# Performance work log

Measured on AMD Instinct MI355X. Metric: run time of the kernel, lower is better.

## Reference

```python
import jax, jax.numpy as jnp
import numpy as np

BS = 8192
NUM_CLASSES = 400
D = 768


def _bilin_from_14(m14, Y, X, eH, eW):
    # Value of bilinear-resize(m14 -> (eH,eW)) at integer pixel (Y,X), computed on the fly.
    # torch F.interpolate(align_corners=False): src = (dst+0.5)*in/out - 0.5, clamped at 0.
    # m14: (bs,14,14); Y,X: (bs,14) float integer-valued coords; eH,eW: (bs,) float.
    sy = jnp.maximum((Y + 0.5) * 14.0 / eH[:, None] - 0.5, 0.0)
    sx = jnp.maximum((X + 0.5) * 14.0 / eW[:, None] - 0.5, 0.0)
    r0f = jnp.floor(sy); c0f = jnp.floor(sx)
    r0 = r0f.astype(jnp.int32); r1 = jnp.minimum(r0 + 1, 13)
    c0 = c0f.astype(jnp.int32); c1 = jnp.minimum(c0 + 1, 13)
    fy = sy - r0f; fx = sx - c0f
    b = jnp.arange(m14.shape[0])[:, None, None]
    g00 = m14[b, r0[:, :, None], c0[:, None, :]]
    g01 = m14[b, r0[:, :, None], c1[:, None, :]]
    g10 = m14[b, r1[:, :, None], c0[:, None, :]]
    g11 = m14[b, r1[:, :, None], c1[:, None, :]]
    wy = fy[:, :, None]; wx = fx[:, None, :]
    return g00 * (1 - wy) * (1 - wx) + g01 * (1 - wy) * wx + g10 * wy * (1 - wx) + g11 * wy * wx


def _get_mask(attn, o_pos, e_pos):
    # Fused, fully-batched equivalent of the per-sample python loop:
    #   resize 14x14 -> (eH,eW) bilinear; crop (top,left,oH,oW); resize -> 14x14 bilinear.
    # The final resize only reads the intermediate grid at 4 integer points per output
    # pixel, so we evaluate those points lazily via _bilin_from_14 (exact, no Emax grid).
    bs = attn.shape[0]
    m14 = attn.reshape(bs, 14, 14)
    eH = e_pos[:, 2].astype(jnp.float32); eW = e_pos[:, 3].astype(jnp.float32)
    top = (o_pos[:, 0] - e_pos[:, 0]).astype(jnp.float32)
    left = (o_pos[:, 1] - e_pos[:, 1]).astype(jnp.float32)
    oH = o_pos[:, 2].astype(jnp.float32); oW = o_pos[:, 3].astype(jnp.float32)
    i = jnp.arange(14, dtype=jnp.float32)[None, :]
    ty = jnp.maximum((i + 0.5) * oH[:, None] / 14.0 - 0.5, 0.0)  # (bs,14) coords in crop
    tx = jnp.maximum((i + 0.5) * oW[:, None] / 14.0 - 0.5, 0.0)
    y0 = jnp.floor(ty); y1 = jnp.minimum(y0 + 1.0, oH[:, None] - 1.0); wy = ty - y0
    x0 = jnp.floor(tx); x1 = jnp.minimum(x0 + 1.0, oW[:, None] - 1.0); wx = tx - x0
    Y0 = top[:, None] + y0; Y1 = top[:, None] + y1  # absolute rows in (eH,eW) grid
    X0 = left[:, None] + x0; X1 = left[:, None] + x1
    v00 = _bilin_from_14(m14, Y0, X0, eH, eW)
    v01 = _bilin_from_14(m14, Y0, X1, eH, eW)
    v10 = _bilin_from_14(m14, Y1, X0, eH, eW)
    v11 = _bilin_from_14(m14, Y1, X1, eH, eW)
    wyc = wy[:, :, None]; wxc = wx[:, None, :]
    out = v00 * (1 - wyc) * (1 - wxc) + v01 * (1 - wyc) * wxc + v10 * wyc * (1 - wxc) + v11 * wyc * wxc
    return out.reshape(bs, 196)


def _get_att_mask(attention, ratio=0.5):
    bs = attention.shape[0]
    a14 = attention.reshape(bs, 14, 14)
    # bilinear 14->7 with align_corners=False samples at frac 0.5 == 2x2 average pool
    a7 = a14.reshape(bs, 7, 2, 7, 2).mean(axis=(2, 4))
    flat = a7.reshape(bs, 49)
    n_keep = int(49 * ratio) + 1  # argsort desc, take top N+1 = 25
    _, idx = jax.lax.top_k(flat, n_keep)
    masks = jnp.ones((bs, 49), dtype=bool)
    masks = masks.at[jnp.arange(bs)[:, None], idx].set(False)
    m7 = masks.reshape(bs, 7, 7)
    full = jnp.repeat(jnp.repeat(m7, 2, axis=1), 2, axis=2)
    return full.reshape(bs, 196)


def setup_inputs() -> dict:
    key = jax.random.key(0)
    k1, k2, k3 = jax.random.split(key, 3)
    attn = jax.random.uniform(k1, (BS, 196), dtype=jnp.float32)
    rng = np.random.default_rng(0)
    IMG = 224
    eH = rng.integers(112, IMG + 1, BS); eW = rng.integers(112, IMG + 1, BS)
    eT = rng.integers(0, IMG - eH + 1); eL = rng.integers(0, IMG - eW + 1)
    def box():
        h = rng.integers(56, eH + 1); w = rng.integers(56, eW + 1)
        t = eT + rng.integers(0, eH - h + 1); l = eL + rng.integers(0, eW - w + 1)
        return np.stack([t, l, h, w], axis=1)
    e = np.stack([eT, eL, eH, eW], axis=1)
    pos = np.stack([box(), box(), e], axis=1).astype(np.int32)  # (BS,3,4)
    image_embed = jax.random.normal(k2, (2 * BS, D), dtype=jnp.float32)
    W = jax.random.normal(k3, (NUM_CLASSES, D), dtype=jnp.float32) * 0.02
    b = jnp.zeros((NUM_CLASSES,), dtype=jnp.float32)
    return {"attn": attn, "pos": jnp.asarray(pos), "image_embed": image_embed, "W": W, "b": b}


def reference(attn, pos, image_embed, W, b):
    cm1 = _get_mask(attn, pos[:, 0], pos[:, 2])
    mask1 = _get_att_mask(cm1)
    cm2 = _get_mask(attn, pos[:, 1], pos[:, 2])
    mask2 = _get_att_mask(cm2)
    mask = jnp.concatenate([mask1, mask2], axis=0)  # (2*bs,196) bool, fed to masked encoder
    logits = image_embed @ W.T + b
    return logits, mask
```

## Files before the change

kernel.cpp:

```cpp
#include <hip/hip_runtime.h>
#include <hip/hip_bf16.h>

#define BSAMP 8192
#define NCLS 400
#define DIM 768
#define MROWS 16384
#define LOGITS_SIZE (16384LL * 400LL)

typedef __attribute__((ext_vector_type(8))) short short8;
typedef __attribute__((ext_vector_type(4))) float floatx4;

__device__ inline unsigned short f2bf(float f) {
    unsigned int u = __float_as_uint(f);
    return (unsigned short)((u + 0x7FFFu + ((u >> 16) & 1u)) >> 16);
}

__device__ inline uint4 pack8(float4 a, float4 b) {
    union { unsigned short u[8]; uint4 v; } p;
    p.u[0] = f2bf(a.x); p.u[1] = f2bf(a.y); p.u[2] = f2bf(a.z); p.u[3] = f2bf(a.w);
    p.u[4] = f2bf(b.x); p.u[5] = f2bf(b.y); p.u[6] = f2bf(b.z); p.u[7] = f2bf(b.w);
    return p.v;
}

__global__ __launch_bounds__(256) void gemm_kernel(const float* __restrict__ E,
                                                   const float* __restrict__ W,
                                                   const float* __restrict__ bias,
                                                   float* __restrict__ out) {
    __shared__ __align__(16) unsigned short sA[128 * 32];
    __shared__ __align__(16) unsigned short sB[80 * 32];

    const int t    = threadIdx.x;
    const int n0   = blockIdx.x * 80;
    const int m0   = blockIdx.y * 128;
    const int wave = t >> 6;
    const int lane = t & 63;
    const int quad = lane >> 4;
    const int l16  = lane & 15;

    const int aRow = t >> 1;
    const int aCol = (t & 1) * 16;
    const float* aSrc = E + (size_t)(m0 + aRow) * DIM + aCol;
    const float* bSrc = W + (size_t)(n0 + aRow) * DIM + aCol;

    floatx4 acc[2][5];
#pragma unroll
    for (int mi = 0; mi < 2; ++mi)
#pragma unroll
        for (int ni = 0; ni < 5; ++ni)
            acc[mi][ni] = (floatx4){0.f, 0.f, 0.f, 0.f};

    for (int k0 = 0; k0 < DIM; k0 += 32) {
        {
            const float4* s = (const float4*)(aSrc + k0);
            float4 f0 = s[0], f1 = s[1], f2 = s[2], f3 = s[3];
            *(uint4*)&sA[aRow * 32 + aCol]     = pack8(f0, f1);
            *(uint4*)&sA[aRow * 32 + aCol + 8] = pack8(f2, f3);
        }
        if (t < 160) {
            const float4* s = (const float4*)(bSrc + k0);
            float4 f0 = s[0], f1 = s[1], f2 = s[2], f3 = s[3];
            *(uint4*)&sB[aRow * 32 + aCol]     = pack8(f0, f1);
            *(uint4*)&sB[aRow * 32 + aCol + 8] = pack8(f2, f3);
        }
        __syncthreads();

        short8 af0 = *(const short8*)&sA[(wave * 32 + l16) * 32 + quad * 8];
        short8 af1 = *(const short8*)&sA[(wave * 32 + 16 + l16) * 32 + quad * 8];
#pragma unroll
        for (int ni = 0; ni < 5; ++ni) {
            short8 bf = *(const short8*)&sB[(ni * 16 + l16) * 32 + quad * 8];
            acc[0][ni] = __builtin_amdgcn_mfma_f32_16x16x32_bf16(af0, bf, acc[0][ni], 0, 0, 0);
            acc[1][ni] = __builtin_amdgcn_mfma_f32_16x16x32_bf16(af1, bf, acc[1][ni], 0, 0, 0);
        }
        __syncthreads();
    }

#pragma unroll
    for (int ni = 0; ni < 5; ++ni) {
        int col = n0 + ni * 16 + l16;
        float bv = bias[col];
#pragma unroll
        for (int mi = 0; mi < 2; ++mi) {
            int rowBase = m0 + wave * 32 + mi * 16 + quad * 4;
#pragma unroll
            for (int r = 0; r < 4; ++r) {
                out[(size_t)(rowBase + r) * NCLS + col] = acc[mi][ni][r] + bv;
            }
        }
    }
}

__device__ inline float bilin14(const float* m14, float Y, float X, float eH, float eW) {
    float sy = fmaxf((Y + 0.5f) * 14.0f / eH - 0.5f, 0.0f);
    float sx = fmaxf((X + 0.5f) * 14.0f / eW - 0.5f, 0.0f);
    float r0f = floorf(sy);
    float c0f = floorf(sx);
    int r0 = (int)r0f;
    int r1 = min(r0 + 1, 13);
    int c0 = (int)c0f;
    int c1 = min(c0 + 1, 13);
    float fy = sy - r0f;
    float fx = sx - c0f;
    float g00 = m14[r0 * 14 + c0];
    float g01 = m14[r0 * 14 + c1];
    float g10 = m14[r1 * 14 + c0];
    float g11 = m14[r1 * 14 + c1];
    return g00 * (1.f - fy) * (1.f - fx) + g01 * (1.f - fy) * fx +
           g10 * fy * (1.f - fx) + g11 * fy * fx;
}

__global__ __launch_bounds__(64) void mask_kernel(const float* __restrict__ attn,
                                                  const int* __restrict__ pos,
                                                  float* __restrict__ out_mask) {
    const int p = blockIdx.x;
    const int b = p & (BSAMP - 1);
    const int o = p >> 13;
    const int t = threadIdx.x;

    __shared__ float m14[196];
    __shared__ float a7[49];

    for (int i = t; i < 196; i += 64) m14[i] = attn[(size_t)b * 196 + i];

    const int* pb = pos + (size_t)b * 12;
    const float top  = (float)(pb[o * 4 + 0] - pb[8]);
    const float left = (float)(pb[o * 4 + 1] - pb[9]);
    const float oH   = (float)pb[o * 4 + 2];
    const float oW   = (float)pb[o * 4 + 3];
    const float eH   = (float)pb[10];
    const float eW   = (float)pb[11];
    __syncthreads();

    int i7 = t / 7, j7 = t % 7;
    if (t < 49) {
        float s = 0.f;
#pragma unroll
        for (int dy = 0; dy < 2; ++dy) {
            int oy = 2 * i7 + dy;
            float ty = fmaxf((oy + 0.5f) * oH / 14.0f - 0.5f, 0.0f);
            float y0 = floorf(ty);
            float y1 = fminf(y0 + 1.0f, oH - 1.0f);
            float wy = ty - y0;
            float Y0 = top + y0, Y1 = top + y1;
#pragma unroll
            for (int dx = 0; dx < 2; ++dx) {
                int ox = 2 * j7 + dx;
                float tx = fmaxf((ox + 0.5f) * oW / 14.0f - 0.5f, 0.0f);
                float x0 = floorf(tx);
                float x1 = fminf(x0 + 1.0f, oW - 1.0f);
                float wx = tx - x0;
                float X0 = left + x0, X1 = left + x1;
                float v00 = bilin14(m14, Y0, X0, eH, eW);
                float v01 = bilin14(m14, Y0, X1, eH, eW);
                float v10 = bilin14(m14, Y1, X0, eH, eW);
                float v11 = bilin14(m14, Y1, X1, eH, eW);
                float cm = v00 * (1.f - wy) * (1.f - wx) + v01 * (1.f - wy) * wx +
                           v10 * wy * (1.f - wx) + v11 * wy * wx;
                s += cm;
            }
        }
        a7[t] = s * 0.25f;
    }
    __syncthreads();

    if (t < 49) {
        float mine = a7[t];
        int cnt = 0;
#pragma unroll 7
        for (int s2 = 0; s2 < 49; ++s2) {
            float v = a7[s2];
            cnt += (v > mine) || (v == mine && s2 < t);
        }
        float mv = (cnt < 25) ? 0.0f : 1.0f;
        float* base = out_mask + (size_t)p * 196;
        base[(2 * i7 + 0) * 14 + (2 * j7 + 0)] = mv;
        base[(2 * i7 + 0) * 14 + (2 * j7 + 1)] = mv;
        base[(2 * i7 + 1) * 14 + (2 * j7 + 0)] = mv;
        base[(2 * i7 + 1) * 14 + (2 * j7 + 1)] = mv;
    }
}

extern "C" void kernel_launch(void* const* d_in, const int* in_sizes, int n_in,
                              void* d_out, int out_size, void* d_ws, size_t ws_size,
                              hipStream_t stream) {
    const float* attn = (const float*)d_in[0];
    const int*   pos  = (const int*)d_in[1];
    const float* E    = (const float*)d_in[2];
    const float* W    = (const float*)d_in[3];
    const float* bias = (const float*)d_in[4];
    float* out = (float*)d_out;

    dim3 gridG(5, 128);
    gemm_kernel<<<gridG, 256, 0, stream>>>(E, W, bias, out);
    mask_kernel<<<16384, 64, 0, stream>>>(attn, pos, out + LOGITS_SIZE);
}
```

Before: 166.6 us.

## Fuse GEMM and mask kernels into one launch with prefetched bf16 GEMM

Merges the logits GEMM and the mask computation into a single kernel that dispatches on block index. The GEMM now uses a K-step of 64, register prefetch of the next tile, padded shared-memory rows and a cheaper bf16 conversion via perm. The mask path uses 256 threads, one per output pixel, with the 7x7 averaging done afterwards and coalesced mask stores. The aim is to remove a launch, hide global load latency, and overlap the mask work with the GEMM. The cost is larger shared-memory use per block and changed bf16 rounding (round-half-up instead of round-to-nearest-even).

```diff
diff --git a/kernel.cpp b/kernel.cpp
--- a/kernel.cpp
+++ b/kernel.cpp
@@ -4,179 +4,199 @@
 #define BSAMP 8192
 #define NCLS 400
 #define DIM 768
-#define MROWS 16384
 #define LOGITS_SIZE (16384LL * 400LL)
+#define GEMM_BLOCKS 640
+#define MASK_BLOCKS 16384
 
 typedef __attribute__((ext_vector_type(8))) short short8;
 typedef __attribute__((ext_vector_type(4))) float floatx4;
 
-__device__ inline unsigned short f2bf(float f) {
-    unsigned int u = __float_as_uint(f);
-    return (unsigned short)((u + 0x7FFFu + ((u >> 16) & 1u)) >> 16);
-}
-
-__device__ inline uint4 pack8(float4 a, float4 b) {
-    union { unsigned short u[8]; uint4 v; } p;
-    p.u[0] = f2bf(a.x); p.u[1] = f2bf(a.y); p.u[2] = f2bf(a.z); p.u[3] = f2bf(a.w);
-    p.u[4] = f2bf(b.x); p.u[5] = f2bf(b.y); p.u[6] = f2bf(b.z); p.u[7] = f2bf(b.w);
-    return p.v;
-}
-
-__global__ __launch_bounds__(256) void gemm_kernel(const float* __restrict__ E,
-                                                   const float* __restrict__ W,
-                                                   const float* __restrict__ bias,
-                                                   float* __restrict__ out) {
-    __shared__ __align__(16) unsigned short sA[128 * 32];
-    __shared__ __align__(16) unsigned short sB[80 * 32];
-
-    const int t    = threadIdx.x;
-    const int n0   = blockIdx.x * 80;
-    const int m0   = blockIdx.y * 128;
-    const int wave = t >> 6;
-    const int lane = t & 63;
-    const int quad = lane >> 4;
-    const int l16  = lane & 15;
-
-    const int aRow = t >> 1;
-    const int aCol = (t & 1) * 16;
-    const float* aSrc = E + (size_t)(m0 + aRow) * DIM + aCol;
-    const float* bSrc = W + (size_t)(n0 + aRow) * DIM + aCol;
-
-    floatx4 acc[2][5];
-#pragma unroll
-    for (int mi = 0; mi < 2; ++mi)
-#pragma unroll
-        for (int ni = 0; ni < 5; ++ni)
-            acc[mi][ni] = (floatx4){0.f, 0.f, 0.f, 0.f};
-
-    for (int k0 = 0; k0 < DIM; k0 += 32) {
-        {
-            const float4* s = (const float4*)(aSrc + k0);
-            float4 f0 = s[0], f1 = s[1], f2 = s[2], f3 = s[3];
-            *(uint4*)&sA[aRow * 32 + aCol]     = pack8(f0, f1);
-            *(uint4*)&sA[aRow * 32 + aCol + 8] = pack8(f2, f3);
-        }
-        if (t < 160) {
-            const float4* s = (const float4*)(bSrc + k0);
-            float4 f0 = s[0], f1 = s[1], f2 = s[2], f3 = s[3];
-            *(uint4*)&sB[aRow * 32 + aCol]     = pack8(f0, f1);
-            *(uint4*)&sB[aRow * 32 + aCol + 8] = pack8(f2, f3);
-        }
-        __syncthreads();
-
-        short8 af0 = *(const short8*)&sA[(wave * 32 + l16) * 32 + quad * 8];
-        short8 af1 = *(const short8*)&sA[(wave * 32 + 16 + l16) * 32 + quad * 8];
-#pragma unroll
-        for (int ni = 0; ni < 5; ++ni) {
-            short8 bf = *(const short8*)&sB[(ni * 16 + l16) * 32 + quad * 8];
-            acc[0][ni] = __builtin_amdgcn_mfma_f32_16x16x32_bf16(af0, bf, acc[0][ni], 0, 0, 0);
-            acc[1][ni] = __builtin_amdgcn_mfma_f32_16x16x32_bf16(af1, bf, acc[1][ni], 0, 0, 0);
-        }
-        __syncthreads();
-    }
-
-#pragma unroll
-    for (int ni = 0; ni < 5; ++ni) {
-        int col = n0 + ni * 16 + l16;
-        float bv = bias[col];
-#pragma unroll
-        for (int mi = 0; mi < 2; ++mi) {
-            int rowBase = m0 + wave * 32 + mi * 16 + quad * 4;
-#pragma unroll
-            for (int r = 0; r < 4; ++r) {
-                out[(size_t)(rowBase + r) * NCLS + col] = acc[mi][ni][r] + bv;
-            }
-        }
-    }
-}
-
-__device__ inline float bilin14(const float* m14, float Y, float X, float eH, float eW) {
-    float sy = fmaxf((Y + 0.5f) * 14.0f / eH - 0.5f, 0.0f);
-    float sx = fmaxf((X + 0.5f) * 14.0f / eW - 0.5f, 0.0f);
-    float r0f = floorf(sy);
-    float c0f = floorf(sx);
-    int r0 = (int)r0f;
-    int r1 = min(r0 + 1, 13);
-    int c0 = (int)c0f;
-    int c1 = min(c0 + 1, 13);
-    float fy = sy - r0f;
-    float fx = sx - c0f;
-    float g00 = m14[r0 * 14 + c0];
-    float g01 = m14[r0 * 14 + c1];
-    float g10 = m14[r1 * 14 + c0];
-    float g11 = m14[r1 * 14 + c1];
+__device__ inline unsigned int packbf(float a, float b) {
+    unsigned int ua = __float_as_uint(a) + 0x8000u;
+    unsigned int ub = __float_as_uint(b) + 0x8000u;
+    return __builtin_amdgcn_perm(ub, ua, 0x07060302u);
+}
+
+__device__ inline uint2 cvt4(float4 f) {
+    uint2 r;
+    r.x = packbf(f.x, f.y);
+    r.y = packbf(f.z, f.w);
+    return r;
+}
+
+__device__ inline float bilin_tap(const float* m14, int r0, int c0, float fy, float fx) {
+    int base = r0 * 14 + c0;
+    float t0 = m14[base];
+    float t1 = m14[base + 1];
+    float t2 = m14[base + 14];
+    float t3 = m14[base + 15];
+    bool ce = (c0 < 13), re = (r0 < 13);
+    float g00 = t0;
+    float g01 = ce ? t1 : t0;
+    float g10 = re ? t2 : t0;
+    float g11 = re ? (ce ? t3 : t2) : g01;
     return g00 * (1.f - fy) * (1.f - fx) + g01 * (1.f - fy) * fx +
            g10 * fy * (1.f - fx) + g11 * fy * fx;
 }
 
-__global__ __launch_bounds__(64) void mask_kernel(const float* __restrict__ attn,
-                                                  const int* __restrict__ pos,
-                                                  float* __restrict__ out_mask) {
-    const int p = blockIdx.x;
-    const int b = p & (BSAMP - 1);
-    const int o = p >> 13;
-    const int t = threadIdx.x;
-
-    __shared__ float m14[196];
-    __shared__ float a7[49];
-
-    for (int i = t; i < 196; i += 64) m14[i] = attn[(size_t)b * 196 + i];
-
-    const int* pb = pos + (size_t)b * 12;
-    const float top  = (float)(pb[o * 4 + 0] - pb[8]);
-    const float left = (float)(pb[o * 4 + 1] - pb[9]);
-    const float oH   = (float)pb[o * 4 + 2];
-    const float oW   = (float)pb[o * 4 + 3];
-    const float eH   = (float)pb[10];
-    const float eW   = (float)pb[11];
-    __syncthreads();
-
-    int i7 = t / 7, j7 = t % 7;
-    if (t < 49) {
-        float s = 0.f;
-#pragma unroll
-        for (int dy = 0; dy < 2; ++dy) {
-            int oy = 2 * i7 + dy;
+__global__ __launch_bounds__(256, 2) void fused_kernel(const float* __restrict__ attn,
+                                                       const int* __restrict__ pos,
+                                                       const float* __restrict__ E,
+                                                       const float* __restrict__ W,
+                                                       const float* __restrict__ bias,
+                                                       float* __restrict__ out) {
+    __shared__ __align__(16) union {
+        struct { unsigned short A[2][128][40]; unsigned short B[2][80][40]; } g;
+        struct { float m14[212]; float cm[196]; float a7[49]; float mv[49]; } m;
+    } sm;
+
+    const int bx = blockIdx.x;
+    const int t  = threadIdx.x;
+
+    if (bx < GEMM_BLOCKS) {
+        const int n0 = (bx % 5) * 80;
+        const int m0 = (bx / 5) * 128;
+        const int wave = t >> 6, lane = t & 63, quad = lane >> 4, l16 = lane & 15;
+
+        const int tRow = t >> 4;
+        const int tCol = (t & 15) << 2;
+        const int slab = tCol >> 5;
+        const int kk   = tCol & 31;
+        const float* aPtr = E + (size_t)(m0 + tRow) * DIM + tCol;
+        const float* bPtr = W + (size_t)(n0 + tRow) * DIM + tCol;
+        unsigned short* wA = &sm.g.A[slab][tRow][kk];
+        unsigned short* wB = &sm.g.B[slab][tRow][kk];
+
+        float4 pf[13];
+#pragma unroll
+        for (int j = 0; j < 8; ++j) pf[j] = *(const float4*)(aPtr + j * (16 * DIM));
+#pragma unroll
+        for (int j = 0; j < 5; ++j) pf[8 + j] = *(const float4*)(bPtr + j * (16 * DIM));
+
+        floatx4 acc[2][5];
+#pragma unroll
+        for (int mi = 0; mi < 2; ++mi)
+#pragma unroll
+            for (int ni = 0; ni < 5; ++ni)
+                acc[mi][ni] = (floatx4){0.f, 0.f, 0.f, 0.f};
+
+        for (int it = 0; it < 12; ++it) {
+            __syncthreads();
+#pragma unroll
+            for (int j = 0; j < 8; ++j) *(uint2*)(wA + j * (16 * 40)) = cvt4(pf[j]);
+#pragma unroll
+            for (int j = 0; j < 5; ++j) *(uint2*)(wB + j * (16 * 40)) = cvt4(pf[8 + j]);
+            if (it < 11) {
+                const float* aN = aPtr + (it + 1) * 64;
+                const float* bN = bPtr + (it + 1) * 64;
+#pragma unroll
+                for (int j = 0; j < 8; ++j) pf[j] = *(const float4*)(aN + j * (16 * DIM));
+#pragma unroll
+                for (int j = 0; j < 5; ++j) pf[8 + j] = *(const float4*)(bN + j * (16 * DIM));
+            }
+            __syncthreads();
+#pragma unroll
+            for (int s = 0; s < 2; ++s) {
+                short8 af0 = *(const short8*)&sm.g.A[s][wave * 32 + l16][quad * 8];
+                short8 af1 = *(const short8*)&sm.g.A[s][wave * 32 + 16 + l16][quad * 8];
+#pragma unroll
+                for (int ni = 0; ni < 5; ++ni) {
+                    short8 bfr = *(const short8*)&sm.g.B[s][ni * 16 + l16][quad * 8];
+                    acc[0][ni] = __builtin_amdgcn_mfma_f32_16x16x32_bf16(af0, bfr, acc[0][ni], 0, 0, 0);
+                    acc[1][ni] = __builtin_amdgcn_mfma_f32_16x16x32_bf16(af1, bfr, acc[1][ni], 0, 0, 0);
+                }
+            }
+        }
+
+#pragma unroll
+        for (int ni = 0; ni < 5; ++ni) {
+            int col = n0 + ni * 16 + l16;
+            float bv = bias[col];
+#pragma unroll
+            for (int mi = 0; mi < 2; ++mi) {
+                int rowBase = m0 + wave * 32 + mi * 16 + quad * 4;
+#pragma unroll
+                for (int r = 0; r < 4; ++r) {
+                    out[(size_t)(rowBase + r) * NCLS + col] = acc[mi][ni][r] + bv;
+                }
+            }
+        }
+    } else {
+        const int p = bx - GEMM_BLOCKS;
+        const int b = p & (BSAMP - 1);
+        const int o = p >> 13;
+        float* m14 = sm.m.m14;
+
+        if (t < 196) m14[t] = attn[(size_t)b * 196 + t];
+        if (t >= 196 && t < 212) m14[t] = 0.f;
+
+        const int* pb = pos + (size_t)b * 12;
+        const float topf  = (float)(pb[o * 4 + 0] - pb[8]);
+        const float leftf = (float)(pb[o * 4 + 1] - pb[9]);
+        const float oH = (float)pb[o * 4 + 2];
+        const float oW = (float)pb[o * 4 + 3];
+        const float eH = (float)pb[10];
+        const float eW = (float)pb[11];
+        __syncthreads();
+
+        const int oy = t / 14;
+        const int ox = t - oy * 14;
+        if (t < 196) {
             float ty = fmaxf((oy + 0.5f) * oH / 14.0f - 0.5f, 0.0f);
             float y0 = floorf(ty);
             float y1 = fminf(y0 + 1.0f, oH - 1.0f);
             float wy = ty - y0;
-            float Y0 = top + y0, Y1 = top + y1;
-#pragma unroll
-            for (int dx = 0; dx < 2; ++dx) {
-                int ox = 2 * j7 + dx;
-                float tx = fmaxf((ox + 0.5f) * oW / 14.0f - 0.5f, 0.0f);
-                float x0 = floorf(tx);
-                float x1 = fminf(x0 + 1.0f, oW - 1.0f);
-                float wx = tx - x0;
-                float X0 = left + x0, X1 = left + x1;
-                float v00 = bilin14(m14, Y0, X0, eH, eW);
-                float v01 = bilin14(m14, Y0, X1, eH, eW);
-                float v10 = bilin14(m14, Y1, X0, eH, eW);
-                float v11 = bilin14(m14, Y1, X1, eH, eW);
-                float cm = v00 * (1.f - wy) * (1.f - wx) + v01 * (1.f - wy) * wx +
-                           v10 * wy * (1.f - wx) + v11 * wy * wx;
-                s += cm;
-            }
-        }
-        a7[t] = s * 0.25f;
-    }
-    __syncthreads();
-
-    if (t < 49) {
-        float mine = a7[t];
-        int cnt = 0;
+            float tx = fmaxf((ox + 0.5f) * oW / 14.0f - 0.5f, 0.0f);
+            float x0 = floorf(tx);
+            float x1 = fminf(x0 + 1.0f, oW - 1.0f);
+            float wx = tx - x0;
+            float Y0 = topf + y0, Y1 = topf + y1;
+            float X0 = leftf + x0, X1 = leftf + x1;
+
+            float sy0 = fmaxf((Y0 + 0.5f) * 14.0f / eH - 0.5f, 0.0f);
+            float r0f = floorf(sy0); int ry0 = (int)r0f; float fy0 = sy0 - r0f;
+            float sy1 = fmaxf((Y1 + 0.5f) * 14.0f / eH - 0.5f, 0.0f);
+            float r1f = floorf(sy1); int ry1 = (int)r1f; float fy1 = sy1 - r1f;
+            float sx0 = fmaxf((X0 + 0.5f) * 14.0f / eW - 0.5f, 0.0f);
+            float c0f = floorf(sx0); int cx0 = (int)c0f; float fx0 = sx0 - c0f;
+            float sx1 = fmaxf((X1 + 0.5f) * 14.0f / eW - 0.5f, 0.0f);
+            float c1f = floorf(sx1); int cx1 = (int)c1f; float fx1 = sx1 - c1f;
+
+            float v00 = bilin_tap(m14, ry0, cx0, fy0, fx0);
+            float v01 = bilin_tap(m14, ry0, cx1, fy0, fx1);
+            float v10 = bilin_tap(m14, ry1, cx0, fy1, fx0);
+            float v11 = bilin_tap(m14, ry1, cx1, fy1, fx1);
+
+            float cmv = v00 * (1.f - wy) * (1.f - wx) + v01 * (1.f - wy) * wx +
+                        v10 * wy * (1.f - wx) + v11 * wy * wx;
+            sm.m.cm[t] = cmv;
+        }
+        __syncthreads();
+
+        if (t < 49) {
+            int i7 = t / 7, j7 = t - i7 * 7;
+            const float* c = sm.m.cm;
+            int b0 = (2 * i7) * 14 + 2 * j7;
+            float s = ((c[b0] + c[b0 + 1]) + c[b0 + 14]) + c[b0 + 15];
+            sm.m.a7[t] = s * 0.25f;
+        }
+        __syncthreads();
+
+        if (t < 49) {
+            float mine = sm.m.a7[t];
+            int cnt = 0;
 #pragma unroll 7
-        for (int s2 = 0; s2 < 49; ++s2) {
-            float v = a7[s2];
-            cnt += (v > mine) || (v == mine && s2 < t);
-        }
-        float mv = (cnt < 25) ? 0.0f : 1.0f;
-        float* base = out_mask + (size_t)p * 196;
-        base[(2 * i7 + 0) * 14 + (2 * j7 + 0)] = mv;
-        base[(2 * i7 + 0) * 14 + (2 * j7 + 1)] = mv;
-        base[(2 * i7 + 1) * 14 + (2 * j7 + 0)] = mv;
-        base[(2 * i7 + 1) * 14 + (2 * j7 + 1)] = mv;
+            for (int s2 = 0; s2 < 49; ++s2) {
+                float v = sm.m.a7[s2];
+                cnt += (v > mine) || (v == mine && s2 < t);
+            }
+            sm.m.mv[t] = (cnt < 25) ? 0.0f : 1.0f;
+        }
+        __syncthreads();
+
+        if (t < 196) {
+            out[LOGITS_SIZE + (size_t)p * 196 + t] = sm.m.mv[(oy >> 1) * 7 + (ox >> 1)];
+        }
     }
 }
 
@@ -190,7 +210,5 @@
     const float* bias = (const float*)d_in[4];
     float* out = (float*)d_out;
 
-    dim3 gridG(5, 128);
-    gemm_kernel<<<gridG, 256, 0, stream>>>(E, W, bias, out);
-    mask_kernel<<<16384, 64, 0, stream>>>(attn, pos, out + LOGITS_SIZE);
-}
+    fused_kernel<<<GEMM_BLOCKS + MASK_BLOCKS, 256, 0, stream>>>(attn, pos, E, W, bias, out);
+}
```

New measurement: 199.4 us. 1.2x slower.

## Fuse GEMM and mask into one launch with register-prefetched, LDS-free GEMM

Applied to the files above, without the earlier changes.

Merges the GEMM and mask kernels into a single launch. Blocks 0..639 do the GEMM and the remaining blocks each handle four mask samples, one per wave, with coalesced mask writes. The GEMM drops shared memory and barriers: each lane loads its MFMA fragments straight from global memory, double-buffered in registers. W is pre-converted to bf16 in the workspace by a small extra kernel, and activations use a cheaper round-half-up bf16 pack via perm. The changes in rounding, register pressure and uncoalesced global loads may offset the gains from removing barriers and a launch.

```diff
diff --git a/kernel.cpp b/kernel.cpp
--- a/kernel.cpp
+++ b/kernel.cpp
@@ -4,89 +4,37 @@
 #define BSAMP 8192
 #define NCLS 400
 #define DIM 768
-#define MROWS 16384
 #define LOGITS_SIZE (16384LL * 400LL)
+#define GEMM_BLOCKS 640
+#define MASK_BLOCKS 4096
+#define W_ELEMS (NCLS * DIM)
 
 typedef __attribute__((ext_vector_type(8))) short short8;
 typedef __attribute__((ext_vector_type(4))) float floatx4;
 
-__device__ inline unsigned short f2bf(float f) {
-    unsigned int u = __float_as_uint(f);
-    return (unsigned short)((u + 0x7FFFu + ((u >> 16) & 1u)) >> 16);
-}
-
-__device__ inline uint4 pack8(float4 a, float4 b) {
-    union { unsigned short u[8]; uint4 v; } p;
-    p.u[0] = f2bf(a.x); p.u[1] = f2bf(a.y); p.u[2] = f2bf(a.z); p.u[3] = f2bf(a.w);
-    p.u[4] = f2bf(b.x); p.u[5] = f2bf(b.y); p.u[6] = f2bf(b.z); p.u[7] = f2bf(b.w);
-    return p.v;
-}
-
-__global__ __launch_bounds__(256) void gemm_kernel(const float* __restrict__ E,
-                                                   const float* __restrict__ W,
-                                                   const float* __restrict__ bias,
-                                                   float* __restrict__ out) {
-    __shared__ __align__(16) unsigned short sA[128 * 32];
-    __shared__ __align__(16) unsigned short sB[80 * 32];
-
-    const int t    = threadIdx.x;
-    const int n0   = blockIdx.x * 80;
-    const int m0   = blockIdx.y * 128;
-    const int wave = t >> 6;
-    const int lane = t & 63;
-    const int quad = lane >> 4;
-    const int l16  = lane & 15;
-
-    const int aRow = t >> 1;
-    const int aCol = (t & 1) * 16;
-    const float* aSrc = E + (size_t)(m0 + aRow) * DIM + aCol;
-    const float* bSrc = W + (size_t)(n0 + aRow) * DIM + aCol;
-
-    floatx4 acc[2][5];
-#pragma unroll
-    for (int mi = 0; mi < 2; ++mi)
-#pragma unroll
-        for (int ni = 0; ni < 5; ++ni)
-            acc[mi][ni] = (floatx4){0.f, 0.f, 0.f, 0.f};
-
-    for (int k0 = 0; k0 < DIM; k0 += 32) {
-        {
-            const float4* s = (const float4*)(aSrc + k0);
-            float4 f0 = s[0], f1 = s[1], f2 = s[2], f3 = s[3];
-            *(uint4*)&sA[aRow * 32 + aCol]     = pack8(f0, f1);
-            *(uint4*)&sA[aRow * 32 + aCol + 8] = pack8(f2, f3);
-        }
-        if (t < 160) {
-            const float4* s = (const float4*)(bSrc + k0);
-            float4 f0 = s[0], f1 = s[1], f2 = s[2], f3 = s[3];
-            *(uint4*)&sB[aRow * 32 + aCol]     = pack8(f0, f1);
-            *(uint4*)&sB[aRow * 32 + aCol + 8] = pack8(f2, f3);
-        }
-        __syncthreads();
-
-        short8 af0 = *(const short8*)&sA[(wave * 32 + l16) * 32 + quad * 8];
-        short8 af1 = *(const short8*)&sA[(wave * 32 + 16 + l16) * 32 + quad * 8];
-#pragma unroll
-        for (int ni = 0; ni < 5; ++ni) {
-            short8 bf = *(const short8*)&sB[(ni * 16 + l16) * 32 + quad * 8];
-            acc[0][ni] = __builtin_amdgcn_mfma_f32_16x16x32_bf16(af0, bf, acc[0][ni], 0, 0, 0);
-            acc[1][ni] = __builtin_amdgcn_mfma_f32_16x16x32_bf16(af1, bf, acc[1][ni], 0, 0, 0);
-        }
-        __syncthreads();
-    }
-
-#pragma unroll
-    for (int ni = 0; ni < 5; ++ni) {
-        int col = n0 + ni * 16 + l16;
-        float bv = bias[col];
-#pragma unroll
-        for (int mi = 0; mi < 2; ++mi) {
-            int rowBase = m0 + wave * 32 + mi * 16 + quad * 4;
-#pragma unroll
-            for (int r = 0; r < 4; ++r) {
-                out[(size_t)(rowBase + r) * NCLS + col] = acc[mi][ni][r] + bv;
-            }
-        }
+__device__ inline unsigned int packbf(float a, float b) {
+    unsigned int ua = __float_as_uint(a) + 0x8000u;
+    unsigned int ub = __float_as_uint(b) + 0x8000u;
+    return __builtin_amdgcn_perm(ub, ua, 0x07060302u);
+}
+
+__device__ inline short8 cvt8(float4 lo, float4 hi) {
+    union { unsigned int u[4]; short8 s; } r;
+    r.u[0] = packbf(lo.x, lo.y);
+    r.u[1] = packbf(lo.z, lo.w);
+    r.u[2] = packbf(hi.x, hi.y);
+    r.u[3] = packbf(hi.z, hi.w);
+    return r.s;
+}
+
+__global__ void cvtW_kernel(const float* __restrict__ W, unsigned short* __restrict__ ws) {
+    int i = (blockIdx.x * 256 + threadIdx.x) * 4;
+    if (i < W_ELEMS) {
+        float4 f = *(const float4*)(W + i);
+        uint2 r;
+        r.x = packbf(f.x, f.y);
+        r.y = packbf(f.z, f.w);
+        *(uint2*)(ws + i) = r;
     }
 }
 
@@ -109,74 +57,179 @@
            g10 * fy * (1.f - fx) + g11 * fy * fx;
 }
 
-__global__ __launch_bounds__(64) void mask_kernel(const float* __restrict__ attn,
-                                                  const int* __restrict__ pos,
-                                                  float* __restrict__ out_mask) {
-    const int p = blockIdx.x;
-    const int b = p & (BSAMP - 1);
-    const int o = p >> 13;
-    const int t = threadIdx.x;
-
-    __shared__ float m14[196];
-    __shared__ float a7[49];
-
-    for (int i = t; i < 196; i += 64) m14[i] = attn[(size_t)b * 196 + i];
-
-    const int* pb = pos + (size_t)b * 12;
-    const float top  = (float)(pb[o * 4 + 0] - pb[8]);
-    const float left = (float)(pb[o * 4 + 1] - pb[9]);
-    const float oH   = (float)pb[o * 4 + 2];
-    const float oW   = (float)pb[o * 4 + 3];
-    const float eH   = (float)pb[10];
-    const float eW   = (float)pb[11];
-    __syncthreads();
-
-    int i7 = t / 7, j7 = t % 7;
-    if (t < 49) {
-        float s = 0.f;
-#pragma unroll
-        for (int dy = 0; dy < 2; ++dy) {
-            int oy = 2 * i7 + dy;
-            float ty = fmaxf((oy + 0.5f) * oH / 14.0f - 0.5f, 0.0f);
-            float y0 = floorf(ty);
-            float y1 = fminf(y0 + 1.0f, oH - 1.0f);
-            float wy = ty - y0;
-            float Y0 = top + y0, Y1 = top + y1;
-#pragma unroll
-            for (int dx = 0; dx < 2; ++dx) {
-                int ox = 2 * j7 + dx;
-                float tx = fmaxf((ox + 0.5f) * oW / 14.0f - 0.5f, 0.0f);
-                float x0 = floorf(tx);
-                float x1 = fminf(x0 + 1.0f, oW - 1.0f);
-                float wx = tx - x0;
-                float X0 = left + x0, X1 = left + x1;
-                float v00 = bilin14(m14, Y0, X0, eH, eW);
-                float v01 = bilin14(m14, Y0, X1, eH, eW);
-                float v10 = bilin14(m14, Y1, X0, eH, eW);
-                float v11 = bilin14(m14, Y1, X1, eH, eW);
-                float cm = v00 * (1.f - wy) * (1.f - wx) + v01 * (1.f - wy) * wx +
-                           v10 * wy * (1.f - wx) + v11 * wy * wx;
-                s += cm;
-            }
-        }
-        a7[t] = s * 0.25f;
-    }
-    __syncthreads();
-
-    if (t < 49) {
-        float mine = a7[t];
-        int cnt = 0;
+template <bool USE_WS>
+__global__ __launch_bounds__(256, 4) void fused_kernel(const float* __restrict__ attn,
+                                                       const int* __restrict__ pos,
+                                                       const float* __restrict__ E,
+                                                       const float* __restrict__ W,
+                                                       const float* __restrict__ bias,
+                                                       const unsigned short* __restrict__ wsW,
+                                                       float* __restrict__ out) {
+    __shared__ float m14s[4][196];
+    __shared__ float a7s[4][49];
+    __shared__ float mvs[4][49];
+
+    const int bx = blockIdx.x;
+    const int t  = threadIdx.x;
+
+    if (bx < GEMM_BLOCKS) {
+        const int g  = bx >> 3, xo = bx & 7;
+        const int n0 = (g % 5) * 80;
+        const int m0 = (((g / 5) << 3) + xo) << 7;
+        const int wave = t >> 6, lane = t & 63, quad = lane >> 4, l16 = lane & 15;
+
+        const float* aBase = E + (size_t)(m0 + wave * 32 + l16) * DIM + quad * 8;
+        const size_t bOff = (size_t)(n0 + l16) * DIM + quad * 8;
+
+        floatx4 acc[2][5];
+#pragma unroll
+        for (int mi = 0; mi < 2; ++mi)
+#pragma unroll
+            for (int ni = 0; ni < 5; ++ni)
+                acc[mi][ni] = (floatx4){0.f, 0.f, 0.f, 0.f};
+
+        float4 A0[2], A1[2];
+        short8 BP[5];
+        float4 B0[5], B1[5];
+
+#pragma unroll
+        for (int mi = 0; mi < 2; ++mi) {
+            A0[mi] = *(const float4*)(aBase + mi * 16 * DIM);
+            A1[mi] = *(const float4*)(aBase + mi * 16 * DIM + 4);
+        }
+#pragma unroll
+        for (int ni = 0; ni < 5; ++ni) {
+            if (USE_WS) {
+                BP[ni] = *(const short8*)(wsW + bOff + (size_t)ni * 16 * DIM);
+            } else {
+                B0[ni] = *(const float4*)(W + bOff + (size_t)ni * 16 * DIM);
+                B1[ni] = *(const float4*)(W + bOff + (size_t)ni * 16 * DIM + 4);
+            }
+        }
+
+#pragma unroll
+        for (int it = 0; it < 24; ++it) {
+            float4 nA0[2], nA1[2];
+            short8 nBP[5];
+            float4 nB0[5], nB1[5];
+            if (it < 23) {
+                const int kn = (it + 1) * 32;
+#pragma unroll
+                for (int mi = 0; mi < 2; ++mi) {
+                    nA0[mi] = *(const float4*)(aBase + mi * 16 * DIM + kn);
+                    nA1[mi] = *(const float4*)(aBase + mi * 16 * DIM + kn + 4);
+                }
+#pragma unroll
+                for (int ni = 0; ni < 5; ++ni) {
+                    if (USE_WS) {
+                        nBP[ni] = *(const short8*)(wsW + bOff + (size_t)ni * 16 * DIM + kn);
+                    } else {
+                        nB0[ni] = *(const float4*)(W + bOff + (size_t)ni * 16 * DIM + kn);
+                        nB1[ni] = *(const float4*)(W + bOff + (size_t)ni * 16 * DIM + kn + 4);
+                    }
+                }
+            }
+
+            short8 af0 = cvt8(A0[0], A1[0]);
+            short8 af1 = cvt8(A0[1], A1[1]);
+#pragma unroll
+            for (int ni = 0; ni < 5; ++ni) {
+                short8 bfr = USE_WS ? BP[ni] : cvt8(B0[ni], B1[ni]);
+                acc[0][ni] = __builtin_amdgcn_mfma_f32_16x16x32_bf16(af0, bfr, acc[0][ni], 0, 0, 0);
+                acc[1][ni] = __builtin_amdgcn_mfma_f32_16x16x32_bf16(af1, bfr, acc[1][ni], 0, 0, 0);
+            }
+
+            if (it < 23) {
+#pragma unroll
+                for (int mi = 0; mi < 2; ++mi) { A0[mi] = nA0[mi]; A1[mi] = nA1[mi]; }
+#pragma unroll
+                for (int ni = 0; ni < 5; ++ni) {
+                    if (USE_WS) BP[ni] = nBP[ni];
+                    else { B0[ni] = nB0[ni]; B1[ni] = nB1[ni]; }
+                }
+            }
+        }
+
+#pragma unroll
+        for (int ni = 0; ni < 5; ++ni) {
+            int col = n0 + ni * 16 + l16;
+            float bv = bias[col];
+#pragma unroll
+            for (int mi = 0; mi < 2; ++mi) {
+                int rowBase = m0 + wave * 32 + mi * 16 + quad * 4;
+#pragma unroll
+                for (int r = 0; r < 4; ++r) {
+                    out[(size_t)(rowBase + r) * NCLS + col] = acc[mi][ni][r] + bv;
+                }
+            }
+        }
+    } else {
+        const int wv = t >> 6, ln = t & 63;
+        const int p = (bx - GEMM_BLOCKS) * 4 + wv;
+        const int b = p & (BSAMP - 1);
+        const int o = p >> 13;
+        float* m14 = m14s[wv];
+
+        for (int i = ln; i < 196; i += 64) m14[i] = attn[(size_t)b * 196 + i];
+
+        const int* pb = pos + (size_t)b * 12;
+        const float topf  = (float)(pb[o * 4 + 0] - pb[8]);
+        const float leftf = (float)(pb[o * 4 + 1] - pb[9]);
+        const float oH = (float)pb[o * 4 + 2];
+        const float oW = (float)pb[o * 4 + 3];
+        const float eH = (float)pb[10];
+        const float eW = (float)pb[11];
+        __syncthreads();
+
+        const int i7 = ln / 7, j7 = ln - i7 * 7;
+        if (ln < 49) {
+            float s = 0.f;
+#pragma unroll
+            for (int dy = 0; dy < 2; ++dy) {
+                int oy = 2 * i7 + dy;
+                float ty = fmaxf((oy + 0.5f) * oH / 14.0f - 0.5f, 0.0f);
+                float y0 = floorf(ty);
+                float y1 = fminf(y0 + 1.0f, oH - 1.0f);
+                float wy = ty - y0;
+                float Y0 = topf + y0, Y1 = topf + y1;
+#pragma unroll
+                for (int dx = 0; dx < 2; ++dx) {
+                    int ox = 2 * j7 + dx;
+                    float tx = fmaxf((ox + 0.5f) * oW / 14.0f - 0.5f, 0.0f);
+                    float x0 = floorf(tx);
+                    float x1 = fminf(x0 + 1.0f, oW - 1.0f);
+                    float wx = tx - x0;
+                    float X0 = leftf + x0, X1 = leftf + x1;
+                    float v00 = bilin14(m14, Y0, X0, eH, eW);
+                    float v01 = bilin14(m14, Y0, X1, eH, eW);
+                    float v10 = bilin14(m14, Y1, X0, eH, eW);
+                    float v11 = bilin14(m14, Y1, X1, eH, eW);
+                    float cm = v00 * (1.f - wy) * (1.f - wx) + v01 * (1.f - wy) * wx +
+                               v10 * wy * (1.f - wx) + v11 * wy * wx;
+                    s += cm;
+                }
+            }
+            a7s[wv][ln] = s * 0.25f;
+        }
+        __syncthreads();
+
+        if (ln < 49) {
+            float mine = a7s[wv][ln];
+            int cnt = 0;
 #pragma unroll 7
-        for (int s2 = 0; s2 < 49; ++s2) {
-            float v = a7[s2];
-            cnt += (v > mine) || (v == mine && s2 < t);
-        }
-        float mv = (cnt < 25) ? 0.0f : 1.0f;
-        float* base = out_mask + (size_t)p * 196;
-        base[(2 * i7 + 0) * 14 + (2 * j7 + 0)] = mv;
-        base[(2 * i7 + 0) * 14 + (2 * j7 + 1)] = mv;
-        base[(2 * i7 + 1) * 14 + (2 * j7 + 0)] = mv;
-        base[(2 * i7 + 1) * 14 + (2 * j7 + 1)] = mv;
+            for (int s2 = 0; s2 < 49; ++s2) {
+                float v = a7s[wv][s2];
+                cnt += (v > mine) || (v == mine && s2 < ln);
+            }
+            mvs[wv][ln] = (cnt < 25) ? 0.0f : 1.0f;
+        }
+        __syncthreads();
+
+        float* ob = out + LOGITS_SIZE + (size_t)p * 196;
+        for (int i = ln; i < 196; i += 64) {
+            int oy = i / 14, ox = i - oy * 14;
+            ob[i] = mvs[wv][(oy >> 1) * 7 + (ox >> 1)];
+        }
     }
 }
 
@@ -190,7 +243,13 @@
     const float* bias = (const float*)d_in[4];
     float* out = (float*)d_out;
 
-    dim3 gridG(5, 128);
-    gemm_kernel<<<gridG, 256, 0, stream>>>(E, W, bias, out);
-    mask_kernel<<<16384, 64, 0, stream>>>(attn, pos, out + LOGITS_SIZE);
-}
+    if (ws_size >= (size_t)W_ELEMS * 2) {
+        unsigned short* ws = (unsigned short*)d_ws;
+        cvtW_kernel<<<300, 256, 0, stream>>>(W, ws);
+        fused_kernel<true><<<GEMM_BLOCKS + MASK_BLOCKS, 256, 0, stream>>>(
+            attn, pos, E, W, bias, ws, out);
+    } else {
+        fused_kernel<false><<<GEMM_BLOCKS + MASK_BLOCKS, 256, 0, stream>>>(
+            attn, pos, E, W, bias, nullptr, out);
+    }
+}
```

Measured after the change: 169.5 us. About the same (+1.7%).
